# Kernel optimization log

Measured on AMD Instinct MI355X. Metric: run time of the kernel, lower is better.

The kernel has to match this reference:

```python
import jax, jax.numpy as jnp
import numpy as np

TAU = 10.0
EPS = 1e-6
TOP_K = 8


def setup_inputs() -> dict:
    key = jax.random.key(0)
    ks = jax.random.split(key, 5)
    D, NB, H = 1024, 512, 4096
    B, S = 4, 2048
    x = jax.random.normal(ks[0], (B, S, D), dtype=jnp.float32)
    W1 = jax.random.normal(ks[1], (H, D), dtype=jnp.float32) * (1.0 / np.sqrt(D))
    W2 = jax.random.normal(ks[2], (D, H), dtype=jnp.float32) * (1.0 / np.sqrt(H))
    ln_g = jnp.ones((D,), jnp.float32)
    ln_b = jnp.zeros((D,), jnp.float32)
    router_W = jax.random.normal(ks[3], (NB, D), dtype=jnp.float32) * 0.01
    router_b = jnp.zeros((NB,), jnp.float32)
    raw_U = jax.random.normal(ks[4], (NB, D), dtype=jnp.float32) * 0.02
    raw_V = jax.random.normal(jax.random.fold_in(key, 7), (NB, D), dtype=jnp.float32) * 0.02
    gamma = jnp.ones((1, 1, D), jnp.float32) * 0.1
    return {"x": x, "W1": W1, "W2": W2, "ln_g": ln_g, "ln_b": ln_b,
            "router_W": router_W, "router_b": router_b,
            "raw_U": raw_U, "raw_V": raw_V, "gamma": gamma}


def _layernorm(x, g, b):
    mu = jnp.mean(x, axis=-1, keepdims=True)
    var = jnp.var(x, axis=-1, keepdims=True)
    return (x - mu) * jax.lax.rsqrt(var + 1e-5) * g + b


def _unit_rows(W):
    n = jnp.linalg.norm(W, axis=1, keepdims=True)
    return W / jnp.maximum(n, EPS)


def reference(x, W1, W2, ln_g, ln_b, router_W, router_b, raw_U, raw_V, gamma):
    B, S, D = x.shape
    x_flat = x.reshape(-1, D)                      # [N, D]
    r_raw = _layernorm(x_flat, ln_g, ln_b) @ router_W.T + router_b  # [N, NB]
    r = jnp.clip(r_raw, -TAU, TAU)
    alpha = jax.nn.softplus(r)
    phi, idx = jax.lax.top_k(alpha, TOP_K)         # [N, K]
    S_sum = jnp.sum(phi, axis=-1, keepdims=True)
    Z = (phi / (S_sum + EPS)) * jnp.tanh(S_sum)    # [N, K]
    U_sel = _unit_rows(raw_U)[idx]                 # [N, K, D]
    V_sel = _unit_rows(raw_V)[idx]                 # [N, K, D]
    h_lat = jnp.einsum('nd,nkd->nk', x_flat, U_sel)
    dyn = jnp.einsum('nk,nkd->nd', h_lat * Z, V_sel).reshape(B, S, D) * gamma
    static = (jax.nn.gelu(x_flat @ W1.T, approximate=False) @ W2.T).reshape(B, S, D)
    return static + dyn
```

## Files before the change

kernel.cpp:

```cpp
#include <hip/hip_runtime.h>
#include <hip/hip_bf16.h>
#include <math.h>

#define N_TOK 8192
#define DDIM  1024
#define HDIM  4096
#define NBLK  512

typedef __bf16 bf16x8 __attribute__((ext_vector_type(8)));
typedef __bf16 bf16x4 __attribute__((ext_vector_type(4)));
typedef float  floatx4 __attribute__((ext_vector_type(4)));

__device__ __forceinline__ float wave_reduce_sum(float v) {
#pragma unroll
    for (int off = 32; off > 0; off >>= 1) v += __shfl_down(v, off, 64);
    return v;
}

__device__ __forceinline__ void gload_lds16(const void* g, void* l) {
    __builtin_amdgcn_global_load_lds((const __attribute__((address_space(1))) void*)g,
                                     (__attribute__((address_space(3))) void*)l,
                                     16, 0, 0);
}

__device__ __forceinline__ float fast_gelu(float x) {
    float ax = fabsf(x);
    float z  = ax * 0.70710678118654752f;
    float t  = __builtin_amdgcn_rcpf(fmaf(0.3275911f, z, 1.0f));
    float p  = fmaf(fmaf(fmaf(fmaf(1.061405429f, t, -1.453152027f),
                              t, 1.421413741f),
                         t, -0.284496736f),
                    t, 0.254829592f);
    p *= t;
    float e = __expf(-z * z);
    float E = fmaf(-p, e, 1.0f);
    return 0.5f * fmaf(ax, E, x);
}

__device__ __forceinline__ float fast_softplus(float r) {
    return __logf(fmaf(1.0f, __expf(r), 1.0f));
}

__device__ __forceinline__ void cast1024(const float* __restrict__ s,
                                         __bf16* __restrict__ d,
                                         size_t off, int t) {
    float4 v = ((const float4*)(s + off))[t];
    bf16x4 o;
    o.x = (__bf16)v.x; o.y = (__bf16)v.y;
    o.z = (__bf16)v.z; o.w = (__bf16)v.w;
    ((bf16x4*)(d + off))[t] = o;
}

__global__ __launch_bounds__(256) void prep_kernel(
        const float* __restrict__ x,
        const float* __restrict__ ln_g, const float* __restrict__ ln_b,
        const float* __restrict__ W1,   const float* __restrict__ W2,
        const float* __restrict__ router_W,
        const float* __restrict__ rawU, const float* __restrict__ rawV,
        __bf16* __restrict__ xb,  __bf16* __restrict__ lnb,
        __bf16* __restrict__ w1b, __bf16* __restrict__ w2b,
        __bf16* __restrict__ rwb,
        float* __restrict__ unitU, float* __restrict__ unitV) {
    int b = blockIdx.x;
    int t = threadIdx.x;

    if (b < 1024) {
        const float* src = (b < NBLK) ? rawU + (size_t)b * DDIM
                                      : rawV + (size_t)(b - NBLK) * DDIM;
        float* dst = (b < NBLK) ? unitU + (size_t)b * DDIM
                                : unitV + (size_t)(b - NBLK) * DDIM;
        float vals[4];
        float ss = 0.f;
#pragma unroll
        for (int i = 0; i < 4; i++) { vals[i] = src[t + i * 256]; ss += vals[i] * vals[i]; }
        __shared__ float red[4];
        ss = wave_reduce_sum(ss);
        if ((t & 63) == 0) red[t >> 6] = ss;
        __syncthreads();
        float tot = red[0] + red[1] + red[2] + red[3];
        float inv = 1.f / fmaxf(sqrtf(tot), 1e-6f);
#pragma unroll
        for (int i = 0; i < 4; i++) dst[t + i * 256] = vals[i] * inv;
    } else if (b < 9216) {
        int n = b - 1024;
        const float* row = x + (size_t)n * DDIM;
        float v[4];
        float s1 = 0.f, s2 = 0.f;
#pragma unroll
        for (int i = 0; i < 4; i++) {
            v[i] = row[t + i * 256];
            s1 += v[i];
            s2 += v[i] * v[i];
        }
        __shared__ float r1[4], r2[4];
        s1 = wave_reduce_sum(s1);
        s2 = wave_reduce_sum(s2);
        if ((t & 63) == 0) { r1[t >> 6] = s1; r2[t >> 6] = s2; }
        __syncthreads();
        float mu  = (r1[0] + r1[1] + r1[2] + r1[3]) * (1.f / DDIM);
        float var = (r2[0] + r2[1] + r2[2] + r2[3]) * (1.f / DDIM) - mu * mu;
        float rstd = rsqrtf(var + 1e-5f);
        __bf16* orow = lnb + (size_t)n * DDIM;
        __bf16* xrow = xb  + (size_t)n * DDIM;
#pragma unroll
        for (int i = 0; i < 4; i++) {
            int d = t + i * 256;
            orow[d] = (__bf16)((v[i] - mu) * rstd * ln_g[d] + ln_b[d]);
            xrow[d] = (__bf16)v[i];
        }
    } else if (b < 13312) {
        cast1024(W1, w1b, (size_t)(b - 9216) * 1024, t);
    } else if (b < 17408) {
        cast1024(W2, w2b, (size_t)(b - 13312) * 1024, t);
    } else {
        cast1024(router_W, rwb, (size_t)(b - 17408) * 1024, t);
    }
}

template <int MODE>
__global__ __launch_bounds__(256) void mfma_gemm(const __bf16* __restrict__ A,
                                                 const __bf16* __restrict__ B,
                                                 const float* __restrict__ bias,
                                                 void* __restrict__ Cv,
                                                 int M, int Nn, int Kk) {
    __shared__ __align__(16) __bf16 As[2][128 * 32];
    __shared__ __align__(16) __bf16 Bs[2][128 * 32];

    const int t    = threadIdx.x;
    const int lane = t & 63;
    const int wave = t >> 6;
    const int wm   = wave >> 1, wn = wave & 1;
    const int lr   = lane & 15, quad = lane >> 4;
    const int m0   = blockIdx.x * 128;
    const int n0   = blockIdx.y * 128;

    const int kLen  = Kk / gridDim.z;
    const int kBase = blockIdx.z * kLen;

    const int ca0 = t & 3;
    const __bf16* Ag[2];
    const __bf16* Bg[2];
    int ldsOff[2];
#pragma unroll
    for (int q = 0; q < 2; q++) {
        int idx = q * 256 + t;
        Ag[q]     = A + (size_t)(m0 + (idx >> 2)) * Kk + kBase + ca0 * 8;
        Bg[q]     = B + (size_t)(n0 + (idx >> 2)) * Kk + kBase + ca0 * 8;
        ldsOff[q] = idx * 8;
    }

    int raOff[4], rbOff[4];
#pragma unroll
    for (int i = 0; i < 4; i++) {
        raOff[i] = (wm * 64 + i * 16 + lr) * 32 + quad * 8;
        rbOff[i] = (wn * 64 + i * 16 + lr) * 32 + quad * 8;
    }

    floatx4 acc[4][4];
#pragma unroll
    for (int i = 0; i < 4; i++)
#pragma unroll
        for (int j = 0; j < 4; j++) acc[i][j] = (floatx4)0.f;

#pragma unroll
    for (int q = 0; q < 2; q++) {
        gload_lds16(Ag[q], &As[0][ldsOff[q]]);
        gload_lds16(Bg[q], &Bs[0][ldsOff[q]]);
    }

    const int niter = kLen >> 5;
    for (int it = 0; it < niter; ++it) {
        const int cur = it & 1;
        __syncthreads();
        if (it + 1 < niter) {
            const int nk = (it + 1) << 5;
            const int nb = cur ^ 1;
#pragma unroll
            for (int q = 0; q < 2; q++) {
                gload_lds16(Ag[q] + nk, &As[nb][ldsOff[q]]);
                gload_lds16(Bg[q] + nk, &Bs[nb][ldsOff[q]]);
            }
        }
        bf16x8 af[4], bfr[4];
#pragma unroll
        for (int i = 0; i < 4; i++) af[i]  = *(const bf16x8*)&As[cur][raOff[i]];
#pragma unroll
        for (int j = 0; j < 4; j++) bfr[j] = *(const bf16x8*)&Bs[cur][rbOff[j]];
#pragma unroll
        for (int i = 0; i < 4; i++)
#pragma unroll
            for (int j = 0; j < 4; j++)
                acc[i][j] = __builtin_amdgcn_mfma_f32_16x16x32_bf16(af[i], bfr[j],
                                                                    acc[i][j], 0, 0, 0);
    }

    const int mBase = m0 + wm * 64 + quad * 4;
    const int nBase = n0 + wn * 64 + lr;
#pragma unroll
    for (int i = 0; i < 4; i++) {
#pragma unroll
        for (int j = 0; j < 4; j++) {
            int n = nBase + j * 16;
#pragma unroll
            for (int r = 0; r < 4; r++) {
                int m = mBase + i * 16 + r;
                float v = acc[i][j][r];
                if (MODE == 0) {
                    float rr = v + bias[n];
                    rr = fminf(fmaxf(rr, -10.f), 10.f);
                    ((float*)Cv)[(size_t)m * Nn + n] = fast_softplus(rr);
                } else if (MODE == 1) {
                    ((__bf16*)Cv)[(size_t)m * Nn + n] = (__bf16)fast_gelu(v);
                } else {
                    unsafeAtomicAdd(&((float*)Cv)[(size_t)m * Nn + n], v);
                }
            }
        }
    }
}

__global__ __launch_bounds__(256) void topk_dyn_kernel(
        const float* __restrict__ alpha,
        const float* __restrict__ x,
        const float* __restrict__ unitU,
        const float* __restrict__ unitV,
        const float* __restrict__ gamma,
        float* __restrict__ out) {
    int n = blockIdx.x;
    int t = threadIdx.x;
    int lane = t & 63, wid = t >> 6;

    __shared__ int   sidx[8];
    __shared__ float shz[8];
    __shared__ float red[8][4];
    __shared__ float hz[8];

    if (wid == 0) {
        const float* row = alpha + (size_t)n * NBLK;
        float v[8];
#pragma unroll
        for (int i = 0; i < 8; i++) v[i] = row[lane + i * 64];
        float topv[8];
        int   topi[8];
        for (int s = 0; s < 8; s++) {
            float bv = v[0]; int bi = 0;
#pragma unroll
            for (int i = 1; i < 8; i++)
                if (v[i] > bv) { bv = v[i]; bi = i; }
            int gidx = lane + bi * 64;
#pragma unroll
            for (int off = 1; off < 64; off <<= 1) {
                float ov = __shfl_xor(bv, off, 64);
                int   oi = __shfl_xor(gidx, off, 64);
                if (ov > bv || (ov == bv && oi < gidx)) { bv = ov; gidx = oi; }
            }
            topv[s] = bv; topi[s] = gidx;
            if ((gidx & 63) == lane) v[gidx >> 6] = -1e30f;
        }
        float S = 0.f;
#pragma unroll
        for (int s = 0; s < 8; s++) S += topv[s];
        float zscale = tanhf(S) / (S + 1e-6f);
        if (lane < 8) {
            sidx[lane] = topi[lane];
            shz[lane]  = topv[lane] * zscale;
        }
    }
    __syncthreads();

    const float* xr = x + (size_t)n * DDIM;
    float xv[4];
#pragma unroll
    for (int i = 0; i < 4; i++) xv[i] = xr[t + i * 256];

    float acc[8];
#pragma unroll
    for (int k = 0; k < 8; k++) {
        const float* ur = unitU + (size_t)sidx[k] * DDIM;
        float a = 0.f;
#pragma unroll
        for (int i = 0; i < 4; i++) a = fmaf(xv[i], ur[t + i * 256], a);
        acc[k] = a;
    }
#pragma unroll
    for (int k = 0; k < 8; k++) {
        float a = wave_reduce_sum(acc[k]);
        if (lane == 0) red[k][wid] = a;
    }
    __syncthreads();
    if (t < 8) {
        float h = red[t][0] + red[t][1] + red[t][2] + red[t][3];
        hz[t] = h * shz[t];
    }
    __syncthreads();

    float* orow = out + (size_t)n * DDIM;
#pragma unroll
    for (int i = 0; i < 4; i++) {
        int d = t + i * 256;
        float s = 0.f;
#pragma unroll
        for (int k = 0; k < 8; k++)
            s = fmaf(hz[k], unitV[(size_t)sidx[k] * DDIM + d], s);
        orow[d] = s * gamma[d];
    }
}

extern "C" void kernel_launch(void* const* d_in, const int* in_sizes, int n_in,
                              void* d_out, int out_size, void* d_ws, size_t ws_size,
                              hipStream_t stream) {
    const float* x        = (const float*)d_in[0];
    const float* W1       = (const float*)d_in[1];
    const float* W2       = (const float*)d_in[2];
    const float* ln_g     = (const float*)d_in[3];
    const float* ln_b     = (const float*)d_in[4];
    const float* router_W = (const float*)d_in[5];
    const float* router_b = (const float*)d_in[6];
    const float* raw_U    = (const float*)d_in[7];
    const float* raw_V    = (const float*)d_in[8];
    const float* gamma    = (const float*)d_in[9];
    float* out = (float*)d_out;

    char* ws = (char*)d_ws;
    __bf16* lnb   = (__bf16*)(ws);
    float*  alpha = (float*)(ws + 16777216u);
    __bf16* g1    = (__bf16*)(ws);
    __bf16* xb    = (__bf16*)(ws + 67108864u);
    __bf16* w1b   = (__bf16*)(ws + 83886080u);
    __bf16* w2b   = (__bf16*)(ws + 92274688u);
    __bf16* rwb   = (__bf16*)(ws + 100663296u);
    float*  unitU = (float*)(ws + 101711872u);
    float*  unitV = (float*)(ws + 103809024u);

    prep_kernel<<<17920, 256, 0, stream>>>(x, ln_g, ln_b, W1, W2, router_W,
                                           raw_U, raw_V, xb, lnb, w1b, w2b, rwb,
                                           unitU, unitV);

    dim3 gR(N_TOK / 128, NBLK / 128);
    mfma_gemm<0><<<gR, 256, 0, stream>>>(lnb, rwb, router_b, (void*)alpha, N_TOK, NBLK, DDIM);

    topk_dyn_kernel<<<N_TOK, 256, 0, stream>>>(alpha, x, unitU, unitV, gamma, out);

    dim3 g1d(N_TOK / 128, HDIM / 128);
    mfma_gemm<1><<<g1d, 256, 0, stream>>>(xb, w1b, nullptr, (void*)g1, N_TOK, HDIM, DDIM);

    dim3 g2d(N_TOK / 128, DDIM / 128, 2);
    mfma_gemm<2><<<g2d, 256, 0, stream>>>(g1, w2b, nullptr, (void*)out, N_TOK, DDIM, HDIM);
}
```

Before: 403.1 us.

## Split-K the router GEMM and move bias/clip/softplus into the top-k kernel

The router GEMM (N=512) now runs with split-K of 4 and atomic-adds raw logits into a zeroed buffer, giving it more blocks to fill the GPU. Bias add, clamp and softplus move into the top-k kernel and are applied only to the 8 selected values; this relies on clamp plus softplus being monotonic, so the ranking is unchanged. The second FFN GEMM drops split-K and does a plain read-add-write into out instead of atomics. The cost is an extra memset and atomic traffic on the router path, and fewer blocks for the W2 GEMM.

```diff
diff --git a/kernel.cpp b/kernel.cpp
--- a/kernel.cpp
+++ b/kernel.cpp
@@ -117,10 +117,9 @@
     }
 }
 
-template <int MODE>
+template <int MODE, int SPLITK>
 __global__ __launch_bounds__(256) void mfma_gemm(const __bf16* __restrict__ A,
                                                  const __bf16* __restrict__ B,
-                                                 const float* __restrict__ bias,
                                                  void* __restrict__ Cv,
                                                  int M, int Nn, int Kk) {
     __shared__ __align__(16) __bf16 As[2][128 * 32];
@@ -134,8 +133,8 @@
     const int m0   = blockIdx.x * 128;
     const int n0   = blockIdx.y * 128;
 
-    const int kLen  = Kk / gridDim.z;
-    const int kBase = blockIdx.z * kLen;
+    const int kLen  = Kk / SPLITK;
+    const int kBase = (SPLITK == 1) ? 0 : blockIdx.z * kLen;
 
     const int ca0 = t & 3;
     const __bf16* Ag[2];
@@ -206,13 +205,11 @@
                 int m = mBase + i * 16 + r;
                 float v = acc[i][j][r];
                 if (MODE == 0) {
-                    float rr = v + bias[n];
-                    rr = fminf(fmaxf(rr, -10.f), 10.f);
-                    ((float*)Cv)[(size_t)m * Nn + n] = fast_softplus(rr);
+                    unsafeAtomicAdd(&((float*)Cv)[(size_t)m * Nn + n], v);
                 } else if (MODE == 1) {
                     ((__bf16*)Cv)[(size_t)m * Nn + n] = (__bf16)fast_gelu(v);
                 } else {
-                    unsafeAtomicAdd(&((float*)Cv)[(size_t)m * Nn + n], v);
+                    ((float*)Cv)[(size_t)m * Nn + n] += v;
                 }
             }
         }
@@ -220,7 +217,8 @@
 }
 
 __global__ __launch_bounds__(256) void topk_dyn_kernel(
-        const float* __restrict__ alpha,
+        const float* __restrict__ rraw,
+        const float* __restrict__ router_b,
         const float* __restrict__ x,
         const float* __restrict__ unitU,
         const float* __restrict__ unitV,
@@ -236,10 +234,10 @@
     __shared__ float hz[8];
 
     if (wid == 0) {
-        const float* row = alpha + (size_t)n * NBLK;
+        const float* row = rraw + (size_t)n * NBLK;
         float v[8];
 #pragma unroll
-        for (int i = 0; i < 8; i++) v[i] = row[lane + i * 64];
+        for (int i = 0; i < 8; i++) v[i] = row[lane + i * 64] + router_b[lane + i * 64];
         float topv[8];
         int   topi[8];
         for (int s = 0; s < 8; s++) {
@@ -257,13 +255,18 @@
             topv[s] = bv; topi[s] = gidx;
             if ((gidx & 63) == lane) v[gidx >> 6] = -1e30f;
         }
+        float phi[8];
         float S = 0.f;
 #pragma unroll
-        for (int s = 0; s < 8; s++) S += topv[s];
+        for (int s = 0; s < 8; s++) {
+            float rr = fminf(fmaxf(topv[s], -10.f), 10.f);
+            phi[s] = fast_softplus(rr);
+            S += phi[s];
+        }
         float zscale = tanhf(S) / (S + 1e-6f);
         if (lane < 8) {
             sidx[lane] = topi[lane];
-            shz[lane]  = topv[lane] * zscale;
+            shz[lane]  = phi[lane] * zscale;
         }
     }
     __syncthreads();
@@ -336,14 +339,16 @@
                                            raw_U, raw_V, xb, lnb, w1b, w2b, rwb,
                                            unitU, unitV);
 
-    dim3 gR(N_TOK / 128, NBLK / 128);
-    mfma_gemm<0><<<gR, 256, 0, stream>>>(lnb, rwb, router_b, (void*)alpha, N_TOK, NBLK, DDIM);
-
-    topk_dyn_kernel<<<N_TOK, 256, 0, stream>>>(alpha, x, unitU, unitV, gamma, out);
+    hipMemsetAsync((void*)alpha, 0, (size_t)N_TOK * NBLK * 4, stream);
+    dim3 gR(N_TOK / 128, NBLK / 128, 4);
+    mfma_gemm<0, 4><<<gR, 256, 0, stream>>>(lnb, rwb, (void*)alpha, N_TOK, NBLK, DDIM);
+
+    topk_dyn_kernel<<<N_TOK, 256, 0, stream>>>(alpha, router_b, x, unitU, unitV,
+                                               gamma, out);
 
     dim3 g1d(N_TOK / 128, HDIM / 128);
-    mfma_gemm<1><<<g1d, 256, 0, stream>>>(xb, w1b, nullptr, (void*)g1, N_TOK, HDIM, DDIM);
-
-    dim3 g2d(N_TOK / 128, DDIM / 128, 2);
-    mfma_gemm<2><<<g2d, 256, 0, stream>>>(g1, w2b, nullptr, (void*)out, N_TOK, DDIM, HDIM);
-}
+    mfma_gemm<1, 1><<<g1d, 256, 0, stream>>>(xb, w1b, (void*)g1, N_TOK, HDIM, DDIM);
+
+    dim3 g2d(N_TOK / 128, DDIM / 128);
+    mfma_gemm<2, 1><<<g2d, 256, 0, stream>>>(g1, w2b, (void*)out, N_TOK, DDIM, HDIM);
+}
```

Measured after the change: 428.5 us. 6.3% more time.
